# Performance work log

Hardware: AMD Instinct MI355X
Metric: run time of the kernel (lower is better)

## Reference

```python
import jax, jax.numpy as jnp
import numpy as np

K = 8
NEG = -1e16


def setup_inputs() -> dict:
    key = jax.random.key(0)
    inputs = jax.random.normal(key, (1048576, 64), dtype=jnp.float32)
    return {"inputs": inputs}


def reference(inputs) -> jnp.ndarray:
    depth = inputs.shape[1]
    # top-k along last axis (values unused; only indices form the mask)
    _, top_k_indices = jax.lax.top_k(inputs, K)            # [N, K]
    # sum of one-hots -> membership mask [N, depth]
    one_hot = jax.nn.one_hot(top_k_indices, depth, dtype=inputs.dtype)  # [N, K, depth]
    mask = jnp.sum(one_hot, axis=1)                        # [N, depth]
    sparse_inputs = jnp.where(mask > 0.0, inputs, jnp.full_like(inputs, NEG))
    return jax.nn.softmax(sparse_inputs, axis=1)
```

## Files before the change

### kernel.cpp

```cpp
#include <hip/hip_runtime.h>
#include <math.h>


#define D4 16
#define ROWS 32
#define TILE_F4 (ROWS * D4)
#define WAVES 2
#define THREADS (WAVES * 64)

#define LVL(ti) { const float _hi = fmaxf(ti, _a); _a = fminf(ti, _a); ti = _hi; }
#define INSERT(x) { float _a = (x); \
    LVL(t0) LVL(t1) LVL(t2) LVL(t3) LVL(t4) LVL(t5) LVL(t6) \
    t7 = fmaxf(t7, _a); }

#define PROC(x, o) { \
    const int _kgt = ((x) > thr); \
    const int _keq = ((x) == thr) & (quota > 0); \
    quota -= _keq; \
    (o) = (_kgt | _keq) ? __expf((x) - m) * inv : 0.0f; }

__device__ __forceinline__ void gload_lds16(const void* g, void* l) {
    __builtin_amdgcn_global_load_lds(
        (__attribute__((address_space(1))) void*)(g),
        (__attribute__((address_space(3))) void*)(l),
        16, 0, 0);
}

__global__ __launch_bounds__(THREADS)
void topk_softmax_kernel(const float* __restrict__ in,
                         float* __restrict__ out,
                         int ntiles)
{
    __shared__ float4 tile_[WAVES][TILE_F4];

    const int lane = threadIdx.x & 63;
    const int wid  = threadIdx.x >> 6;
    const int w = blockIdx.x * WAVES + wid;
    if (w >= ntiles) return;
    float4* tile = tile_[wid];

    const float4* __restrict__ p = reinterpret_cast<const float4*>(in) + (long long)w * TILE_F4;
    float4* __restrict__ q       = reinterpret_cast<float4*>(out)      + (long long)w * TILE_F4;

    const int g = lane >> 4;
    const int s = lane & 15;

    #pragma unroll
    for (int c = 0; c < 8; ++c) {
        const int r = c * 4 + g;
        const int k = s ^ (r & 15);
        gload_lds16(p + r * 16 + k, tile + c * 64);
    }
    asm volatile("s_waitcnt vmcnt(0)" ::: "memory");

    const int half = lane >> 5;
    const int r    = lane & 31;
    const int kbase = half << 3;
    const int rk = r & 15;
    float4 v[8];
    #pragma unroll
    for (int c = 0; c < 8; ++c) v[c] = tile[r * 16 + ((kbase + c) ^ rk)];

    float t0 = -INFINITY, t1 = -INFINITY, t2 = -INFINITY, t3 = -INFINITY,
          t4 = -INFINITY, t5 = -INFINITY, t6 = -INFINITY, t7 = -INFINITY;
    #pragma unroll
    for (int c = 0; c < 8; ++c) {
        INSERT(v[c].x) INSERT(v[c].y) INSERT(v[c].z) INSERT(v[c].w)
    }

    const float p0 = __shfl_xor(t0, 32), p1 = __shfl_xor(t1, 32),
                p2 = __shfl_xor(t2, 32), p3 = __shfl_xor(t3, 32),
                p4 = __shfl_xor(t4, 32), p5 = __shfl_xor(t5, 32),
                p6 = __shfl_xor(t6, 32), p7 = __shfl_xor(t7, 32);
    const float c0 = fmaxf(t0, p7), c1 = fmaxf(t1, p6), c2 = fmaxf(t2, p5),
                c3 = fmaxf(t3, p4), c4 = fmaxf(t4, p3), c5 = fmaxf(t5, p2),
                c6 = fmaxf(t6, p1), c7 = fmaxf(t7, p0);
    const float m   = fmaxf(t0, p0);
    const float thr = fminf(fminf(fminf(c0, c1), fminf(c2, c3)),
                            fminf(fminf(c4, c5), fminf(c6, c7)));
    const int cnt_gt = (c0 > thr) + (c1 > thr) + (c2 > thr) + (c3 > thr) +
                       (c4 > thr) + (c5 > thr) + (c6 > thr) + (c7 > thr);
    const float sum = __expf(c0 - m) + __expf(c1 - m) + __expf(c2 - m) + __expf(c3 - m) +
                      __expf(c4 - m) + __expf(c5 - m) + __expf(c6 - m) + __expf(c7 - m);
    const float inv = 1.0f / sum;
    const int quota0 = 8 - cnt_gt;

    int ce = 0;
    #pragma unroll
    for (int c = 0; c < 8; ++c)
        ce += (v[c].x == thr) + (v[c].y == thr) + (v[c].z == thr) + (v[c].w == thr);
    const int ce_partner = __shfl_xor(ce, 32);
    int quota = half ? (quota0 - ce_partner) : quota0;

    #pragma unroll
    for (int c = 0; c < 8; ++c) {
        float4 o;
        PROC(v[c].x, o.x) PROC(v[c].y, o.y) PROC(v[c].z, o.z) PROC(v[c].w, o.w)
        tile[r * 16 + ((kbase + c) ^ rk)] = o;
    }
    asm volatile("s_waitcnt lgkmcnt(0)" ::: "memory");

    #pragma unroll
    for (int c = 0; c < 8; ++c) {
        const int rr = c * 4 + g;
        q[c * 64 + lane] = tile[rr * 16 + (s ^ (rr & 15))];
    }
}

__global__ __launch_bounds__(64)
void topk_softmax_tail(const float* __restrict__ in, float* __restrict__ out,
                       long long row0, long long nrows)
{
    const long long row = row0 + threadIdx.x;
    if (row >= nrows) return;
    const float4* __restrict__ p = reinterpret_cast<const float4*>(in) + row * D4;
    float4* __restrict__ q       = reinterpret_cast<float4*>(out)      + row * D4;
    float4 v[D4];
    #pragma unroll
    for (int c = 0; c < D4; ++c) v[c] = p[c];
    float t0 = -INFINITY, t1 = -INFINITY, t2 = -INFINITY, t3 = -INFINITY,
          t4 = -INFINITY, t5 = -INFINITY, t6 = -INFINITY, t7 = -INFINITY;
    #pragma unroll
    for (int c = 0; c < D4; ++c) {
        INSERT(v[c].x) INSERT(v[c].y) INSERT(v[c].z) INSERT(v[c].w)
    }
    const float thr = t7;
    const float m   = t0;
    int quota = 8 - ((t0 > thr) + (t1 > thr) + (t2 > thr) + (t3 > thr) +
                     (t4 > thr) + (t5 > thr) + (t6 > thr));
    const float sum = __expf(t0 - m) + __expf(t1 - m) + __expf(t2 - m) + __expf(t3 - m) +
                      __expf(t4 - m) + __expf(t5 - m) + __expf(t6 - m) + __expf(t7 - m);
    const float inv = 1.0f / sum;
    #pragma unroll
    for (int c = 0; c < D4; ++c) {
        float4 o;
        PROC(v[c].x, o.x) PROC(v[c].y, o.y) PROC(v[c].z, o.z) PROC(v[c].w, o.w)
        q[c] = o;
    }
}

extern "C" void kernel_launch(void* const* d_in, const int* in_sizes, int n_in,
                              void* d_out, int out_size, void* d_ws, size_t ws_size,
                              hipStream_t stream) {
    const float* in = (const float*)d_in[0];
    float* out = (float*)d_out;
    const long long nrows = in_sizes[0] / 64;
    const int ntiles = (int)(nrows / ROWS);
    const long long rem = nrows - (long long)ntiles * ROWS;

    if (ntiles > 0) {
        const int nblocks = (ntiles + WAVES - 1) / WAVES;
        topk_softmax_kernel<<<nblocks, THREADS, 0, stream>>>(in, out, ntiles);
    }
    if (rem > 0) {
        topk_softmax_tail<<<1, 64, 0, stream>>>(in, out, (long long)ntiles * ROWS, nrows);
    }
}
```

Measured before the change: 100.6 us.

## Split each row across four lanes with sorted shuffle merge of top-8

Each wave now handles 16 rows instead of 32, with four lanes per row holding 16 elements each rather than two lanes holding 32. Partial top-8 lists are merged in two shuffle rounds, using a bitonic-style compare-exchange to re-sort between rounds. Tie-counting for the threshold now uses prefix counts from the top-k registers, and values are re-read from LDS instead of kept in registers. The intent is to cut per-lane serial insertion work and register pressure so occupancy can rise, at the cost of extra shuffles, LDS reads and smaller tiles per wave.

```diff
diff --git a/kernel.cpp b/kernel.cpp
--- a/kernel.cpp
+++ b/kernel.cpp
@@ -3,15 +3,17 @@
 
 
 #define D4 16
-#define ROWS 32
+#define ROWS 16
 #define TILE_F4 (ROWS * D4)
-#define WAVES 2
+#define WAVES 4
 #define THREADS (WAVES * 64)
 
 #define LVL(ti) { const float _hi = fmaxf(ti, _a); _a = fminf(ti, _a); ti = _hi; }
 #define INSERT(x) { float _a = (x); \
     LVL(t0) LVL(t1) LVL(t2) LVL(t3) LVL(t4) LVL(t5) LVL(t6) \
     t7 = fmaxf(t7, _a); }
+
+#define CE(a, b) { const float _hi = fmaxf(a, b); b = fminf(a, b); a = _hi; }
 
 #define PROC(x, o) { \
     const int _kgt = ((x) > thr); \
@@ -26,7 +28,7 @@
         16, 0, 0);
 }
 
-__global__ __launch_bounds__(THREADS)
+__global__ __launch_bounds__(THREADS, 8)
 void topk_softmax_kernel(const float* __restrict__ in,
                          float* __restrict__ out,
                          int ntiles)
@@ -46,64 +48,76 @@
     const int s = lane & 15;
 
     #pragma unroll
-    for (int c = 0; c < 8; ++c) {
+    for (int c = 0; c < 4; ++c) {
         const int r = c * 4 + g;
-        const int k = s ^ (r & 15);
-        gload_lds16(p + r * 16 + k, tile + c * 64);
+        gload_lds16(p + r * 16 + (s ^ r), tile + c * 64);
     }
     asm volatile("s_waitcnt vmcnt(0)" ::: "memory");
 
-    const int half = lane >> 5;
-    const int r    = lane & 31;
-    const int kbase = half << 3;
-    const int rk = r & 15;
-    float4 v[8];
-    #pragma unroll
-    for (int c = 0; c < 8; ++c) v[c] = tile[r * 16 + ((kbase + c) ^ rk)];
-
+    const int r2 = lane & 15;
+    const int h  = lane >> 4;
+    const int qb = h * 4;
     float t0 = -INFINITY, t1 = -INFINITY, t2 = -INFINITY, t3 = -INFINITY,
           t4 = -INFINITY, t5 = -INFINITY, t6 = -INFINITY, t7 = -INFINITY;
     #pragma unroll
-    for (int c = 0; c < 8; ++c) {
-        INSERT(v[c].x) INSERT(v[c].y) INSERT(v[c].z) INSERT(v[c].w)
+    for (int j = 0; j < 4; ++j) {
+        const float4 v = tile[r2 * 16 + ((qb + j) ^ r2)];
+        INSERT(v.x) INSERT(v.y) INSERT(v.z) INSERT(v.w)
     }
 
-    const float p0 = __shfl_xor(t0, 32), p1 = __shfl_xor(t1, 32),
-                p2 = __shfl_xor(t2, 32), p3 = __shfl_xor(t3, 32),
-                p4 = __shfl_xor(t4, 32), p5 = __shfl_xor(t5, 32),
-                p6 = __shfl_xor(t6, 32), p7 = __shfl_xor(t7, 32);
-    const float c0 = fmaxf(t0, p7), c1 = fmaxf(t1, p6), c2 = fmaxf(t2, p5),
-                c3 = fmaxf(t3, p4), c4 = fmaxf(t4, p3), c5 = fmaxf(t5, p2),
-                c6 = fmaxf(t6, p1), c7 = fmaxf(t7, p0);
-    const float m   = fmaxf(t0, p0);
-    const float thr = fminf(fminf(fminf(c0, c1), fminf(c2, c3)),
-                            fminf(fminf(c4, c5), fminf(c6, c7)));
-    const int cnt_gt = (c0 > thr) + (c1 > thr) + (c2 > thr) + (c3 > thr) +
-                       (c4 > thr) + (c5 > thr) + (c6 > thr) + (c7 > thr);
-    const float sum = __expf(c0 - m) + __expf(c1 - m) + __expf(c2 - m) + __expf(c3 - m) +
-                      __expf(c4 - m) + __expf(c5 - m) + __expf(c6 - m) + __expf(c7 - m);
+    const float pa0 = __shfl_xor(t0, 16), pa1 = __shfl_xor(t1, 16),
+                pa2 = __shfl_xor(t2, 16), pa3 = __shfl_xor(t3, 16),
+                pa4 = __shfl_xor(t4, 16), pa5 = __shfl_xor(t5, 16),
+                pa6 = __shfl_xor(t6, 16), pa7 = __shfl_xor(t7, 16);
+    float c0 = fmaxf(t0, pa7), c1 = fmaxf(t1, pa6), c2 = fmaxf(t2, pa5),
+          c3 = fmaxf(t3, pa4), c4 = fmaxf(t4, pa3), c5 = fmaxf(t5, pa2),
+          c6 = fmaxf(t6, pa1), c7 = fmaxf(t7, pa0);
+    CE(c0, c4) CE(c1, c5) CE(c2, c6) CE(c3, c7)
+    CE(c0, c2) CE(c1, c3) CE(c4, c6) CE(c5, c7)
+    CE(c0, c1) CE(c2, c3) CE(c4, c5) CE(c6, c7)
+
+    const float pb0 = __shfl_xor(c0, 32), pb1 = __shfl_xor(c1, 32),
+                pb2 = __shfl_xor(c2, 32), pb3 = __shfl_xor(c3, 32),
+                pb4 = __shfl_xor(c4, 32), pb5 = __shfl_xor(c5, 32),
+                pb6 = __shfl_xor(c6, 32), pb7 = __shfl_xor(c7, 32);
+    const float f0 = fmaxf(c0, pb7), f1 = fmaxf(c1, pb6), f2 = fmaxf(c2, pb5),
+                f3 = fmaxf(c3, pb4), f4 = fmaxf(c4, pb3), f5 = fmaxf(c5, pb2),
+                f6 = fmaxf(c6, pb1), f7 = fmaxf(c7, pb0);
+
+    const float m   = fmaxf(c0, pb0);
+    const float thr = fminf(fminf(fminf(f0, f1), fminf(f2, f3)),
+                            fminf(fminf(f4, f5), fminf(f6, f7)));
+    const int cnt_gt = (f0 > thr) + (f1 > thr) + (f2 > thr) + (f3 > thr) +
+                       (f4 > thr) + (f5 > thr) + (f6 > thr) + (f7 > thr);
+    const float sum = __expf(f0 - m) + __expf(f1 - m) + __expf(f2 - m) + __expf(f3 - m) +
+                      __expf(f4 - m) + __expf(f5 - m) + __expf(f6 - m) + __expf(f7 - m);
     const float inv = 1.0f / sum;
-    const int quota0 = 8 - cnt_gt;
 
-    int ce = 0;
-    #pragma unroll
-    for (int c = 0; c < 8; ++c)
-        ce += (v[c].x == thr) + (v[c].y == thr) + (v[c].z == thr) + (v[c].w == thr);
-    const int ce_partner = __shfl_xor(ce, 32);
-    int quota = half ? (quota0 - ce_partner) : quota0;
+    const int ce = (t0 == thr) + (t1 == thr) + (t2 == thr) + (t3 == thr) +
+                   (t4 == thr) + (t5 == thr) + (t6 == thr) + (t7 == thr);
+    const int e1 = __shfl_xor(ce, 16);
+    const int e2 = __shfl_xor(ce, 32);
+    const int e3 = __shfl_xor(e1, 32);
+    const int a0 = (h == 0) ? ce : (h == 1) ? e1 : (h == 2) ? e2 : e3;
+    const int a1 = (h == 1) ? ce : (h == 0) ? e1 : (h == 3) ? e2 : e3;
+    const int a2 = (h == 2) ? ce : (h == 3) ? e1 : (h == 0) ? e2 : e3;
+    const int pre = (h > 0 ? a0 : 0) + (h > 1 ? a1 : 0) + (h > 2 ? a2 : 0);
+    int quota = 8 - cnt_gt - pre;
 
     #pragma unroll
-    for (int c = 0; c < 8; ++c) {
+    for (int j = 0; j < 4; ++j) {
+        const int slot = r2 * 16 + ((qb + j) ^ r2);
+        const float4 v = tile[slot];
         float4 o;
-        PROC(v[c].x, o.x) PROC(v[c].y, o.y) PROC(v[c].z, o.z) PROC(v[c].w, o.w)
-        tile[r * 16 + ((kbase + c) ^ rk)] = o;
+        PROC(v.x, o.x) PROC(v.y, o.y) PROC(v.z, o.z) PROC(v.w, o.w)
+        tile[slot] = o;
     }
     asm volatile("s_waitcnt lgkmcnt(0)" ::: "memory");
 
     #pragma unroll
-    for (int c = 0; c < 8; ++c) {
-        const int rr = c * 4 + g;
-        q[c * 64 + lane] = tile[rr * 16 + (s ^ (rr & 15))];
+    for (int c = 0; c < 4; ++c) {
+        const int r = c * 4 + g;
+        q[c * 64 + lane] = tile[r * 16 + (s ^ r)];
     }
 }
 
```

Result: faster. 98.17 us (-2.4%).
